# Kernel optimization log

Measured on AMD Instinct MI355X. Metric: run time of the kernel, lower is better.

Reference implementation:

```python
import jax, jax.numpy as jnp
import numpy as np


def _gru_cell(x, h, Wih, Whh, bih, bhh):
    # PyTorch GRU cell (seq_len=1): gates ordered r, z, n
    gi = x @ Wih.T + bih
    gh = h @ Whh.T + bhh
    i_r, i_z, i_n = jnp.split(gi, 3, axis=-1)
    h_r, h_z, h_n = jnp.split(gh, 3, axis=-1)
    r = jax.nn.sigmoid(i_r + h_r)
    z = jax.nn.sigmoid(i_z + h_z)
    n = jnp.tanh(i_n + r * h_n)
    return (1.0 - z) * n + z * h


def setup_inputs() -> dict:
    key = jax.random.key(0)
    N, K, n_in, H = 4096, 8, 14, 128
    ks = jax.random.split(key, 24)
    s = 0.05
    inp = {
        "towers": jax.random.normal(ks[0], (N, K, n_in), jnp.float32),
        # E_n encoder (Linear -> tanh -> Linear -> tanh)
        "En_W1": jax.random.normal(ks[1], (H, n_in)) * s,
        "En_b1": jnp.zeros((H,)),
        "En_W2": jax.random.normal(ks[2], (H, H)) * s,
        "En_b2": jnp.zeros((H,)),
        # E_e encoder
        "Ee_W1": jax.random.normal(ks[3], (H, 2 * n_in)) * s,
        "Ee_b1": jnp.zeros((H,)),
        "Ee_W2": jax.random.normal(ks[4], (H, H)) * s,
        "Ee_b2": jnp.zeros((H,)),
        # U_gru (node update), input n_in + H
        "U_Wih": jax.random.normal(ks[5], (3 * H, n_in + H)) * s,
        "U_Whh": jax.random.normal(ks[6], (3 * H, H)) * s,
        "U_bih": jnp.zeros((3 * H,)),
        "U_bhh": jnp.zeros((3 * H,)),
        # M_gru (edge update), input 2*(n_in + H)
        "M_Wih": jax.random.normal(ks[7], (3 * H, 2 * (n_in + H))) * s,
        "M_Whh": jax.random.normal(ks[8], (3 * H, H)) * s,
        "M_bih": jnp.zeros((3 * H,)),
        "M_bhh": jnp.zeros((3 * H,)),
        # G_gru (global update), input 2*H
        "G_Wih": jax.random.normal(ks[9], (3 * H, 2 * H)) * s,
        "G_Whh": jax.random.normal(ks[10], (3 * H, H)) * s,
        "G_bih": jnp.zeros((3 * H,)),
        "G_bhh": jnp.zeros((3 * H,)),
        # output head
        "O_W": jax.random.normal(ks[11], (1, H)) * s,
        "O_b": jnp.zeros((1,)),
        "k": 3,
    }
    return inp


def reference(towers, En_W1, En_b1, En_W2, En_b2, Ee_W1, Ee_b1, Ee_W2, Ee_b2,
              U_Wih, U_Whh, U_bih, U_bhh, M_Wih, M_Whh, M_bih, M_bhh,
              G_Wih, G_Whh, G_bih, G_bhh, O_W, O_b, k):
    N, K, n_in = towers.shape
    H = En_W1.shape[0]
    # node state init: h = E_n(towers)
    h = jnp.tanh(jnp.tanh(towers @ En_W1.T + En_b1) @ En_W2.T + En_b2)  # (N,K,H)
    # edge state init: e_h = E_e(all-pairs concat of towers)
    xi = jnp.broadcast_to(towers[:, :, None, :], (N, K, K, n_in))
    xj = jnp.broadcast_to(towers[:, None, :, :], (N, K, K, n_in))
    xx0 = jnp.concatenate([xi, xj], axis=-1)  # (N,K,K,2*n_in)
    e_h = jnp.tanh(jnp.tanh(xx0 @ Ee_W1.T + Ee_b1) @ Ee_W2.T + Ee_b2)  # (N,K,K,H)
    # mask[i,j] = 1 iff j == i+1 (the nested-loop mask is a shifted identity)
    mask = jnp.eye(K, k=1, dtype=towers.dtype)
    e = e_h
    D = n_in + H
    for _ in range(k):
        # edge_fn: all-pairs concat of [towers, h] fed through GRU cell
        xh = jnp.concatenate([towers, h], axis=-1)  # (N,K,D)
        a = jnp.broadcast_to(xh[:, :, None, :], (N, K, K, D))
        b = jnp.broadcast_to(xh[:, None, :, :], (N, K, K, D))
        exx = jnp.concatenate([a, b], axis=-1).reshape(-1, 2 * D)
        e_h = _gru_cell(exx, e_h.reshape(-1, H), M_Wih, M_Whh, M_bih, M_bhh)
        e = e_h.reshape(N, K, K, H)
        # node_fn: masked sum selects e[:, i, i+1]
        edges = jnp.einsum('nijh,ij->nih', e, mask)  # (N,K,H)
        nx = jnp.concatenate([towers, edges], axis=-1).reshape(-1, D)
        h = _gru_cell(nx, h.reshape(-1, H), U_Wih, U_Whh, U_bih, U_bhh).reshape(N, K, H)
        e_h = e_h  # state carried
    # global_fn
    h_sum = h.sum(axis=1)  # (N,H)
    e_sum = jnp.einsum('nijh,ij->nh', e, mask)  # (N,H)
    gx = jnp.concatenate([h_sum, e_sum], axis=-1)  # (N,2H)
    g = _gru_cell(gx, jnp.zeros((N, H), towers.dtype), G_Wih, G_Whh, G_bih, G_bhh)
    out = jax.nn.sigmoid((g @ O_W.T + O_b).reshape(N))
    return out
```

## Files before the change

kernel.cpp:

```cpp
#include <hip/hip_runtime.h>
#include <hip/hip_bf16.h>

typedef __hip_bfloat16 bf16;
typedef unsigned short ush;
typedef short s16x8 __attribute__((ext_vector_type(8)));
typedef ush u16x4 __attribute__((ext_vector_type(4)));
typedef float f32x4 __attribute__((ext_vector_type(4)));

#define DEV __device__ __forceinline__

DEV float rcp_f(float x) { return __builtin_amdgcn_rcpf(x); }
DEV float sigmoid_f(float x) { return rcp_f(1.f + __expf(-x)); }
DEV float tanh_f(float x) { return 1.f - 2.f * rcp_f(__expf(2.f * x) + 1.f); }

DEV float u2f(ush u) { unsigned int v = ((unsigned int)u) << 16; float f; __builtin_memcpy(&f, &v, 4); return f; }
DEV ush f2u(float f) { bf16 h = __float2bfloat16(f); ush u; __builtin_memcpy(&u, &h, 2); return u; }

DEV f32x4 MFMA(s16x8 a, s16x8 b, f32x4 c) {
  return __builtin_amdgcn_mfma_f32_16x16x32_bf16(a, b, c, 0, 0, 0);
}

DEV s16x8 z8() {
  s16x8 v;
  for (int z = 0; z < 8; ++z) v[z] = 0;
  return v;
}

DEV int swz_idx(int row, int kk) { return row * 32 + (((kk >> 3) ^ ((row >> 1) & 3)) << 3) + (kk & 7); }
DEV int swz_blk(int row, int blk) { return row * 32 + ((blk ^ ((row >> 1) & 3)) << 3); }


__global__ __launch_bounds__(256) void prep_all(
    const float* __restrict__ towers,
    const float* __restrict__ MWih, const float* __restrict__ MWhh,
    const float* __restrict__ UWih, const float* __restrict__ UWhh,
    const float* __restrict__ EnW1, const float* __restrict__ EnW2,
    const float* __restrict__ EeW1, const float* __restrict__ EeW2,
    const float* __restrict__ MBih, const float* __restrict__ MBhh,
    const float* __restrict__ UBih, const float* __restrict__ UBhh,
    const float* __restrict__ GWih, const float* __restrict__ GWhh,
    const float* __restrict__ GBih, const float* __restrict__ GBhh,
    ush* __restrict__ xh, ush* __restrict__ WPQ, ush* __restrict__ WTh,
    ush* __restrict__ WTu, ush* __restrict__ WBen1, ush* __restrict__ WBen2,
    ush* __restrict__ WBee1, ush* __restrict__ WBee2,
    float* __restrict__ biasM, float* __restrict__ biasU,
    float* __restrict__ WT_G, float* __restrict__ biasG, ush* __restrict__ bn2rep)
{
  const int b = blockIdx.x, t = threadIdx.x;
  if (b < 2048) {
    const int idx = b * 256 + t;
    const int row = idx >> 4, kk = idx & 15;
    xh[row * 144 + kk] = f2u(kk < 14 ? towers[row * 14 + kk] : 0.f);
  } else if (b < 2528) {
    const int idx = (b - 2048) * 256 + t;
    const int ck = idx / 24576, rem = idx % 24576, n = rem >> 5, kk = rem & 31;
    const int k = ck * 32 + kk;
    const int half = (n >= 384);
    const int m = n - half * 384;
    const int g = m >> 7, c = m & 127;
    const int row = g * 128 + c;
    int col = -1;
    if (k < 14)                  col = k;
    else if (k >= 16 && k < 144) col = k - 2;
    if (half && col >= 0)        col += 142;
    WPQ[idx] = f2u((col >= 0) ? MWih[row * 284 + col] : 0.f);
  } else if (b < 2720) {
    const int idx = (b - 2528) * 256 + t;
    const int ck = idx / 12288, rem = idx % 12288, n = rem >> 5, kk = rem & 31;
    const int g = n >> 7, c = n & 127;
    WTh[idx] = f2u(MWhh[(g * 128 + c) * 128 + ck * 32 + kk]);
  } else if (b < 3296) {
    const int idx = (b - 2720) * 256 + t;
    const int ck = idx >> 14, n = (idx >> 5) & 511, kk = idx & 31;
    const int k = ck * 32 + kk, gate = n >> 7, c = n & 127;
    float w = 0.f;
    const int row = (gate == 0) ? c : (gate == 1) ? 128 + c : 256 + c;
    if (k < 160) {
      int col = -1;
      if (k < 16)        { if (k < 14) col = k; }
      else if (k < 144)  col = 14 + (k - 16);
      if (gate != 3 && col >= 0) w = UWih[row * 142 + col];
    } else {
      if (gate != 2) w = UWhh[row * 128 + (k - 160)];
    }
    WTu[ck * 16384 + swz_idx(n, kk)] = f2u(w);
  } else if (b < 3312) {
    const int idx = (b - 3296) * 256 + t;
    const int n = (idx >> 5) & 127, kk = idx & 31;
    WBen1[idx] = f2u(kk < 14 ? EnW1[n * 14 + kk] : 0.f);
  } else if (b < 3376) {
    const int idx = (b - 3312) * 256 + t;
    const int ck = idx >> 12, n = (idx >> 5) & 127, kk = idx & 31;
    WBen2[idx] = f2u(EnW2[n * 128 + ck * 32 + kk]);
  } else if (b < 3392) {
    const int idx = (b - 3376) * 256 + t;
    const int n = (idx >> 5) & 127, kk = idx & 31;
    int col = (kk < 16) ? (kk < 14 ? kk : -1) : (kk < 30 ? 14 + (kk - 16) : -1);
    WBee1[idx] = f2u(col >= 0 ? EeW1[n * 28 + col] : 0.f);
    (void)n;
  } else if (b < 3456) {
    const int idx = (b - 3392) * 256 + t;
    const int ck = idx >> 12, n = (idx >> 5) & 127, kk = idx & 31;
    WBee2[idx] = f2u(EeW2[n * 128 + ck * 32 + kk]);
  } else if (b < 3458) {
    const int idx = (b - 3456) * 256 + t;
    const int g = idx >> 7, c = idx & 127;
    float v;
    if (g == 0)      v = MBih[c] + MBhh[c];
    else if (g == 1) v = MBih[128 + c] + MBhh[128 + c];
    else if (g == 2) v = MBih[256 + c];
    else             v = MBhh[256 + c];
    biasM[idx] = v;
  } else if (b < 3460) {
    const int idx = (b - 3458) * 256 + t;
    const int g = idx >> 7, c = idx & 127;
    float v;
    if (g == 0)      v = UBih[c] + UBhh[c];
    else if (g == 1) v = UBih[128 + c] + UBhh[128 + c];
    else if (g == 2) v = UBih[256 + c];
    else             v = UBhh[256 + c];
    biasU[idx] = v;
  } else if (b < 4228) {
    const int idx = (b - 3460) * 256 + t;
    const int kc = idx >> 9, cg = (idx >> 2) & 127, gate = idx & 3;
    const int row = (gate == 0) ? cg : (gate == 1) ? cg + 128 : cg + 256;
    float v = 0.f;
    if (kc < 256) { if (gate != 3) v = GWih[row * 256 + kc]; }
    else          { if (gate != 2) v = GWhh[row * 128 + (kc - 256)]; }
    WT_G[idx] = v;
  } else if (b < 4230) {
    const int idx = (b - 4228) * 256 + t;
    const int cg = idx >> 2, gate = idx & 3;
    float v;
    if (gate == 0)      v = GBih[cg] + GBhh[cg];
    else if (gate == 1) v = GBih[cg + 128] + GBhh[cg + 128];
    else if (gate == 2) v = GBih[cg + 256];
    else                v = GBhh[cg + 256];
    biasG[idx] = v;
  } else {
    const int idx = (b - 4230) * 256 + t;
    bn2rep[idx] = f2u(MBhh[256 + (idx >> 3)]);
  }
}

DEV void pq_phase(ush* As5, const ush* __restrict__ WPQ,
                  const float* __restrict__ biasM, ush* __restrict__ PqT,
                  int rowBase, int lane, int w)
{
  const int quad = lane >> 4, l15 = lane & 15;
  for (int half = 0; half < 2; ++half) {
    f32x4 acc[6][4];
    #pragma unroll
    for (int tl = 0; tl < 6; ++tl)
      #pragma unroll
      for (int rt = 0; rt < 4; ++rt) {
        #pragma unroll
        for (int q = 0; q < 4; ++q) acc[tl][rt][q] = 0.f;
      }
    for (int ck = 0; ck < 5; ++ck) {
      s16x8 af[4];
      #pragma unroll
      for (int rt = 0; rt < 4; ++rt)
        af[rt] = *(const s16x8*)&As5[ck * 2048 + swz_blk(rt * 16 + l15, quad)];
      #pragma unroll
      for (int tl = 0; tl < 6; ++tl) {
        const int n = w * 96 + tl * 16 + l15;
        const s16x8 bf = *(const s16x8*)&WPQ[(ck * 768 + half * 384 + n) * 32 + quad * 8];
        #pragma unroll
        for (int rt = 0; rt < 4; ++rt) acc[tl][rt] = MFMA(af[rt], bf, acc[tl][rt]);
      }
    }
    #pragma unroll
    for (int tl = 0; tl < 6; ++tl) {
      const int col = w * 96 + tl * 16 + l15;
      const float bv = half ? 0.f : biasM[col];
      #pragma unroll
      for (int rt = 0; rt < 4; ++rt) {
        const int row0 = rowBase + rt * 16 + quad * 4;
        const int g = row0 >> 3, n0 = row0 & 7;
        u16x4 wv;
        #pragma unroll
        for (int q = 0; q < 4; ++q) wv[q] = f2u(acc[tl][rt][q] + bv);
        *(u16x4*)&PqT[((size_t)g * 768 + half * 384 + col) * 8 + n0] = wv;
      }
    }
  }
}

DEV void pq_stage_towers(ush* As5, const ush* __restrict__ xh, int rowBase, int t)
{
  const int gm = t >> 2, gb = t & 3, grow = rowBase + gm;
  if (gb < 2) {
    const s16x8 v = *(const s16x8*)(xh + grow * 144 + gb * 8);
    *(s16x8*)&As5[swz_blk(gm, gb)] = v;
  } else {
    *(s16x8*)&As5[4 * 2048 + swz_blk(gm, gb)] = z8();
  }
}

__global__ __launch_bounds__(256, 2) void enc_en_pq(
    ush* __restrict__ xh,
    const ush* __restrict__ WB1, const float* __restrict__ b1,
    const ush* __restrict__ WB2, const float* __restrict__ b2,
    const ush* __restrict__ WPQ, const float* __restrict__ biasM,
    ush* __restrict__ PqT)
{
  __shared__ ush smem[10240];
  ush* A1  = smem;
  ush* Z1  = smem + 1024;
  ush* As5 = smem;
  const int t = threadIdx.x, lane = t & 63, w = t >> 6;
  const int rowBase = blockIdx.x * 64;
  const int quad = lane >> 4, l15 = lane & 15;

  {
    const int gm = t >> 2, gb = t & 3, grow = rowBase + gm;
    s16x8 v = z8();
    if (gb < 2) v = *(const s16x8*)(xh + grow * 144 + gb * 8);
    *(s16x8*)&A1[swz_blk(gm, gb)] = v;
  }
  __syncthreads();

  s16x8 af[4];
  #pragma unroll
  for (int rt = 0; rt < 4; ++rt)
    af[rt] = *(const s16x8*)&A1[swz_blk(rt * 16 + l15, quad)];
  f32x4 acc1[4][2];
  #pragma unroll
  for (int rt = 0; rt < 4; ++rt)
    #pragma unroll
    for (int ct = 0; ct < 2; ++ct) {
      #pragma unroll
      for (int q = 0; q < 4; ++q) acc1[rt][ct][q] = 0.f;
    }
  #pragma unroll
  for (int ct = 0; ct < 2; ++ct) {
    const int n = w * 32 + ct * 16 + l15;
    const s16x8 bf = *(const s16x8*)&WB1[n * 32 + quad * 8];
    #pragma unroll
    for (int rt = 0; rt < 4; ++rt) acc1[rt][ct] = MFMA(af[rt], bf, acc1[rt][ct]);
  }
  #pragma unroll
  for (int ct = 0; ct < 2; ++ct) {
    const int col = w * 32 + ct * 16 + l15;
    const int kk = col & 31;
    #pragma unroll
    for (int rt = 0; rt < 4; ++rt) {
      #pragma unroll
      for (int q = 0; q < 4; ++q) {
        const int m = rt * 16 + quad * 4 + q;
        Z1[w * 2048 + swz_idx(m, kk)] = f2u(tanh_f(acc1[rt][ct][q] + b1[col]));
      }
    }
  }
  __syncthreads();

  f32x4 acc2[4][2];
  #pragma unroll
  for (int rt = 0; rt < 4; ++rt)
    #pragma unroll
    for (int ct = 0; ct < 2; ++ct) {
      #pragma unroll
      for (int q = 0; q < 4; ++q) acc2[rt][ct][q] = 0.f;
    }
  for (int ck2 = 0; ck2 < 4; ++ck2) {
    #pragma unroll
    for (int rt = 0; rt < 4; ++rt)
      af[rt] = *(const s16x8*)&Z1[ck2 * 2048 + swz_blk(rt * 16 + l15, quad)];
    #pragma unroll
    for (int ct = 0; ct < 2; ++ct) {
      const int n = w * 32 + ct * 16 + l15;
      const s16x8 bf = *(const s16x8*)&WB2[(ck2 * 128 + n) * 32 + quad * 8];
      #pragma unroll
      for (int rt = 0; rt < 4; ++rt) acc2[rt][ct] = MFMA(af[rt], bf, acc2[rt][ct]);
    }
  }
  __syncthreads();

  #pragma unroll
  for (int ct = 0; ct < 2; ++ct) {
    const int col = w * 32 + ct * 16 + l15;
    const int k = 16 + col, ck = k >> 5, kk = k & 31;
    #pragma unroll
    for (int rt = 0; rt < 4; ++rt) {
      #pragma unroll
      for (int q = 0; q < 4; ++q) {
        const int r = rt * 16 + quad * 4 + q;
        const ush hv = f2u(tanh_f(acc2[rt][ct][q] + b2[col]));
        xh[(rowBase + r) * 144 + 16 + col] = hv;
        As5[ck * 2048 + swz_idx(r, kk)] = hv;
      }
    }
  }
  pq_stage_towers(As5, xh, rowBase, t);
  __syncthreads();
  pq_phase(As5, WPQ, biasM, PqT, rowBase, lane, w);
}

DEV void edge_sparse_gru(ush* As, ush* __restrict__ eh,
                         const ush* __restrict__ WTh,
                         const ush* __restrict__ PqT,
                         const ush* __restrict__ bn2rep,
                         int G0, int t)
{
  const int lane = t & 63, w = t >> 6;
  const int quad = lane >> 4, l15 = lane & 15;

  f32x4 accR[2][4], accZ[2][4], accN1[2][4], accN2[2][4];
  #pragma unroll
  for (int mt = 0; mt < 2; ++mt)
    #pragma unroll
    for (int nt = 0; nt < 4; ++nt) {
      #pragma unroll
      for (int q = 0; q < 4; ++q) { accR[mt][nt][q] = 0.f; accZ[mt][nt][q] = 0.f; accN1[mt][nt][q] = 0.f; accN2[mt][nt][q] = 0.f; }
    }

  #pragma unroll
  for (int ck = 0; ck < 4; ++ck) {
    s16x8 be[4];
    #pragma unroll
    for (int nt = 0; nt < 4; ++nt)
      be[nt] = *(const s16x8*)&As[ck * 2048 + swz_blk(nt * 16 + l15, quad)];
    #pragma unroll
    for (int mt = 0; mt < 2; ++mt) {
      const int nb = w * 32 + mt * 16 + l15;
      const int ko = quad * 8;
      const s16x8 aR = *(const s16x8*)&WTh[(ck * 384 + nb) * 32 + ko];
      const s16x8 aZ = *(const s16x8*)&WTh[(ck * 384 + 128 + nb) * 32 + ko];
      const s16x8 aN = *(const s16x8*)&WTh[(ck * 384 + 256 + nb) * 32 + ko];
      #pragma unroll
      for (int nt = 0; nt < 4; ++nt) {
        accR[mt][nt]  = MFMA(aR, be[nt], accR[mt][nt]);
        accZ[mt][nt]  = MFMA(aZ, be[nt], accZ[mt][nt]);
        accN2[mt][nt] = MFMA(aN, be[nt], accN2[mt][nt]);
      }
    }
  }

  {
    s16x8 bI = z8();
    const int i0 = l15 & 7, hi = l15 >> 3;
    if (quad == hi)                       bI[i0]     = (short)0x3F80;
    else if (quad == 2 + hi && i0 < 7)    bI[i0 + 1] = (short)0x3F80;
    const int part = quad >> 1;
    #pragma unroll
    for (int p = 0; p < 4; ++p) {
      const ush* base = PqT + ((size_t)(G0 + 2 * p + (quad & 1)) * 768 + part * 384) * 8;
      #pragma unroll
      for (int mt = 0; mt < 2; ++mt) {
        const int c = w * 32 + mt * 16 + l15;
        const s16x8 aR  = *(const s16x8*)&base[(c) * 8];
        const s16x8 aZ  = *(const s16x8*)&base[(128 + c) * 8];
        const s16x8 aN1 = *(const s16x8*)&base[(256 + c) * 8];
        s16x8 aN2 = z8();
        if (part == 0) aN2 = *(const s16x8*)&bn2rep[c * 8];
        accR[mt][p]  = MFMA(aR,  bI, accR[mt][p]);
        accZ[mt][p]  = MFMA(aZ,  bI, accZ[mt][p]);
        accN1[mt][p] = MFMA(aN1, bI, accN1[mt][p]);
        accN2[mt][p] = MFMA(aN2, bI, accN2[mt][p]);
      }
    }
  }

  #pragma unroll
  for (int mt = 0; mt < 2; ++mt) {
    const int hc0 = w * 32 + mt * 16 + quad * 4;
    const int ck2 = hc0 >> 5, kkB = hc0 & 31;
    #pragma unroll
    for (int nt = 0; nt < 4; ++nt) {
      const int erow = nt * 16 + l15;
      const int gg = erow >> 3, i = erow & 7;
      if (i == 7) continue;
      const u16x4 hp4 = *(const u16x4*)&As[ck2 * 2048 + swz_blk(erow, kkB >> 3) + (kkB & 7)];
      u16x4 ov;
      #pragma unroll
      for (int q = 0; q < 4; ++q) {
        const float rg = sigmoid_f(accR[mt][nt][q]);
        const float zg = sigmoid_f(accZ[mt][nt][q]);
        const float nn = tanh_f(accN1[mt][nt][q] + rg * accN2[mt][nt][q]);
        const float hp = u2f(hp4[q]);
        ov[q] = f2u(nn + zg * (hp - nn));
      }
      *(u16x4*)&eh[(size_t)((G0 + gg) * 64 + i * 9 + 1) * 128 + hc0] = ov;
    }
  }
}

__global__ __launch_bounds__(256, 2) void edge_first(
    ush* __restrict__ eh, const ush* __restrict__ WTh,
    const ush* __restrict__ PqT, const ush* __restrict__ bn2rep,
    const ush* __restrict__ xh,
    const ush* __restrict__ WB1, const float* __restrict__ b1,
    const ush* __restrict__ WB2, const float* __restrict__ b2)
{
  __shared__ ush smem[17408];
  ush* As = smem;
  ush* A1 = smem + 8192;
  ush* Z1 = smem + 9216;
  const int t = threadIdx.x, lane = t & 63, w = t >> 6;
  const int G0 = blockIdx.x * 8;
  const int quad = lane >> 4, l15 = lane & 15;

  {
    const int gm = t >> 2, gb = t & 3;
    const int gg = gm >> 3, i = gm & 7;
    const int xi = (G0 + gg) * 8 + i;
    const int xj = (i < 7) ? xi + 1 : xi;
    const s16x8 v = (gb < 2) ? *(const s16x8*)(xh + xi * 144 + gb * 8)
                             : *(const s16x8*)(xh + xj * 144 + (gb - 2) * 8);
    *(s16x8*)&A1[swz_blk(gm, gb)] = v;
  }
  __syncthreads();

  s16x8 af[4];
  #pragma unroll
  for (int rt = 0; rt < 4; ++rt)
    af[rt] = *(const s16x8*)&A1[swz_blk(rt * 16 + l15, quad)];
  f32x4 acc1[4][2];
  #pragma unroll
  for (int rt = 0; rt < 4; ++rt)
    #pragma unroll
    for (int ct = 0; ct < 2; ++ct) {
      #pragma unroll
      for (int q = 0; q < 4; ++q) acc1[rt][ct][q] = 0.f;
    }
  #pragma unroll
  for (int ct = 0; ct < 2; ++ct) {
    const int n = w * 32 + ct * 16 + l15;
    const s16x8 bf = *(const s16x8*)&WB1[n * 32 + quad * 8];
    #pragma unroll
    for (int rt = 0; rt < 4; ++rt) acc1[rt][ct] = MFMA(af[rt], bf, acc1[rt][ct]);
  }
  #pragma unroll
  for (int ct = 0; ct < 2; ++ct) {
    const int col = w * 32 + ct * 16 + l15;
    const int kk = col & 31;
    #pragma unroll
    for (int rt = 0; rt < 4; ++rt) {
      #pragma unroll
      for (int q = 0; q < 4; ++q) {
        const int m = rt * 16 + quad * 4 + q;
        Z1[w * 2048 + swz_idx(m, kk)] = f2u(tanh_f(acc1[rt][ct][q] + b1[col]));
      }
    }
  }
  __syncthreads();

  f32x4 acc2[4][2];
  #pragma unroll
  for (int rt = 0; rt < 4; ++rt)
    #pragma unroll
    for (int ct = 0; ct < 2; ++ct) {
      #pragma unroll
      for (int q = 0; q < 4; ++q) acc2[rt][ct][q] = 0.f;
    }
  for (int ck2 = 0; ck2 < 4; ++ck2) {
    #pragma unroll
    for (int rt = 0; rt < 4; ++rt)
      af[rt] = *(const s16x8*)&Z1[ck2 * 2048 + swz_blk(rt * 16 + l15, quad)];
    #pragma unroll
    for (int ct = 0; ct < 2; ++ct) {
      const int n = w * 32 + ct * 16 + l15;
      const s16x8 bf = *(const s16x8*)&WB2[(ck2 * 128 + n) * 32 + quad * 8];
      #pragma unroll
      for (int rt = 0; rt < 4; ++rt) acc2[rt][ct] = MFMA(af[rt], bf, acc2[rt][ct]);
    }
  }
  #pragma unroll
  for (int ct = 0; ct < 2; ++ct) {
    const int col = w * 32 + ct * 16 + l15;
    const int kk = col & 31;
    #pragma unroll
    for (int rt = 0; rt < 4; ++rt) {
      #pragma unroll
      for (int q = 0; q < 4; ++q) {
        const int r = rt * 16 + quad * 4 + q;
        As[(col >> 5) * 2048 + swz_idx(r, kk)] = f2u(tanh_f(acc2[rt][ct][q] + b2[col]));
      }
    }
  }
  __syncthreads();

  edge_sparse_gru(As, eh, WTh, PqT, bn2rep, G0, t);
}

__global__ __launch_bounds__(256, 2) void edge_last(
    ush* __restrict__ eh, const ush* __restrict__ WTh,
    const ush* __restrict__ PqT, const ush* __restrict__ bn2rep)
{
  __shared__ ush As[8192];
  const int t = threadIdx.x;
  const int G0 = blockIdx.x * 8;

  {
    const int gm = t >> 2, gb = t & 3;
    const int gg = gm >> 3, i = gm & 7;
    const ush* src = eh + (size_t)((G0 + gg) * 64 + i * 9 + 1) * 128;
    #pragma unroll
    for (int ck = 0; ck < 4; ++ck) {
      s16x8 v = z8();
      if (i < 7) v = *(const s16x8*)(src + ck * 32 + gb * 8);
      *(s16x8*)&As[ck * 2048 + swz_blk(gm, gb)] = v;
    }
  }
  __syncthreads();

  edge_sparse_gru(As, eh, WTh, PqT, bn2rep, G0, t);
}

template<int PQ>
__global__ __launch_bounds__(256, 2) void gru_node_pq(
    ush* __restrict__ xh, const ush* __restrict__ eh,
    const ush* __restrict__ WT, const float* __restrict__ bias,
    const ush* __restrict__ WPQ, const float* __restrict__ biasM,
    ush* __restrict__ PqT)
{
  constexpr int NCH = 9, XCH = 5;
  __shared__ ush smem[10240];
  ush* As5 = smem;
  const int t = threadIdx.x, lane = t & 63, w = t >> 6;
  const int rowBase = blockIdx.x * 64;
  const int gm = t >> 2, gb = t & 3, grow = rowBase + gm;
  const int l15 = lane & 15, quad = lane >> 4;

  f32x4 accR[4][2], accZ[4][2], accN1[4][2], accN2[4][2];
  #pragma unroll
  for (int rt = 0; rt < 4; ++rt)
    #pragma unroll
    for (int s = 0; s < 2; ++s) {
      #pragma unroll
      for (int q = 0; q < 4; ++q) { accR[rt][s][q] = 0.f; accZ[rt][s][q] = 0.f; accN1[rt][s][q] = 0.f; accN2[rt][s][q] = 0.f; }
    }

  auto stage = [&](int ck) {
    const int k0 = ck * 32 + gb * 8;
    s16x8 v = z8();
    if (k0 < 16)       v = *(const s16x8*)(xh + grow * 144 + k0);
    else if (k0 < 144) {
      const int i = grow & 7;
      if (i < 7) v = *(const s16x8*)(eh + (size_t)(grow * 8 + i + 1) * 128 + (k0 - 16));
    } else if (k0 >= 160) {
      v = *(const s16x8*)(xh + grow * 144 + 16 + (k0 - 160));
    }
    *(s16x8*)&smem[(ck & 1) * 2048 + swz_blk(gm, gb)] = v;
  };

  stage(0);
  __syncthreads();

  for (int ck = 0; ck < NCH; ++ck) {
    if (ck + 1 < NCH) stage(ck + 1);

    const ush* Wc = WT + ck * 16384;
    const ush* Ac = smem + (ck & 1) * 2048;
    s16x8 af[4];
    #pragma unroll
    for (int rt = 0; rt < 4; ++rt)
      af[rt] = *(const s16x8*)&Ac[swz_blk(rt * 16 + l15, quad)];
    if (ck < XCH) {
      #pragma unroll
      for (int s = 0; s < 2; ++s) {
        const int nb = w * 32 + s * 16 + l15;
        const s16x8 bR = *(const s16x8*)&Wc[swz_blk(0 * 128 + nb, quad)];
        const s16x8 bZ = *(const s16x8*)&Wc[swz_blk(1 * 128 + nb, quad)];
        const s16x8 bN = *(const s16x8*)&Wc[swz_blk(2 * 128 + nb, quad)];
        #pragma unroll
        for (int rt = 0; rt < 4; ++rt) {
          accR[rt][s]  = MFMA(af[rt], bR, accR[rt][s]);
          accZ[rt][s]  = MFMA(af[rt], bZ, accZ[rt][s]);
          accN1[rt][s] = MFMA(af[rt], bN, accN1[rt][s]);
        }
      }
    } else {
      #pragma unroll
      for (int s = 0; s < 2; ++s) {
        const int nb = w * 32 + s * 16 + l15;
        const s16x8 bR = *(const s16x8*)&Wc[swz_blk(0 * 128 + nb, quad)];
        const s16x8 bZ = *(const s16x8*)&Wc[swz_blk(1 * 128 + nb, quad)];
        const s16x8 bN = *(const s16x8*)&Wc[swz_blk(3 * 128 + nb, quad)];
        #pragma unroll
        for (int rt = 0; rt < 4; ++rt) {
          accR[rt][s]  = MFMA(af[rt], bR, accR[rt][s]);
          accZ[rt][s]  = MFMA(af[rt], bZ, accZ[rt][s]);
          accN2[rt][s] = MFMA(af[rt], bN, accN2[rt][s]);
        }
      }
    }
    __syncthreads();
  }

  #pragma unroll
  for (int s = 0; s < 2; ++s) {
    const int hcol = w * 32 + s * 16 + l15;
    const float bR = bias[hcol], bZ = bias[128 + hcol], bN1 = bias[256 + hcol], bN2 = bias[384 + hcol];
    const int k = 16 + hcol, ckh = k >> 5, kkh = k & 31;
    #pragma unroll
    for (int rt = 0; rt < 4; ++rt) {
      #pragma unroll
      for (int q = 0; q < 4; ++q) {
        const int r = rt * 16 + quad * 4 + q;
        const int row = rowBase + r;
        const float hp = u2f(xh[row * 144 + 16 + hcol]);
        const float rg = sigmoid_f(accR[rt][s][q] + bR);
        const float zg = sigmoid_f(accZ[rt][s][q] + bZ);
        const float nn = tanh_f(accN1[rt][s][q] + bN1 + rg * (accN2[rt][s][q] + bN2));
        const ush hv = f2u(nn + zg * (hp - nn));
        xh[row * 144 + 16 + hcol] = hv;
        if (PQ) As5[ckh * 2048 + swz_idx(r, kkh)] = hv;
      }
    }
  }
  if (PQ) {
    pq_stage_towers(As5, xh, rowBase, t);
    __syncthreads();
    pq_phase(As5, WPQ, biasM, PqT, rowBase, lane, w);
  }
}

__global__ __launch_bounds__(256) void sums2(const ush* __restrict__ xh, const ush* __restrict__ eh,
                                             float* __restrict__ hsum, float* __restrict__ esum) {
  const int idx = blockIdx.x * 256 + threadIdx.x;
  const int n = idx >> 7, hh = idx & 127;
  float hs = 0.f, es = 0.f;
  #pragma unroll
  for (int i = 0; i < 8; ++i) hs += u2f(xh[(n * 8 + i) * 144 + 16 + hh]);
  #pragma unroll
  for (int i = 0; i < 7; ++i) es += u2f(eh[(size_t)((n * 8 + i) * 8 + i + 1) * 128 + hh]);
  hsum[idx] = hs;
  esum[idx] = es;
}

__global__ __launch_bounds__(256) void gru_global_out(
    const float* __restrict__ hsum, const float* __restrict__ esum,
    const float* __restrict__ WT, const float* __restrict__ bias,
    const float* __restrict__ OW, const float* __restrict__ Ob,
    float* __restrict__ out)
{
  constexpr int KT = 384;
  __shared__ float4 ATl4[KT * 4];
  __shared__ float4 Bl4[16 * 128];
  __shared__ float gmat[16 * 128];
  __shared__ float red[16 * 4];
  float* ATl = (float*)ATl4;
  const int t = threadIdx.x;
  const int rowBase = blockIdx.x * 16;
  for (int idx = t; idx < KT * 16; idx += 256) {
    const int kc = idx >> 4, r = idx & 15, grow = rowBase + r;
    float v = 0.f;
    if (kc < 128)      v = hsum[grow * 128 + kc];
    else if (kc < 256) v = esum[grow * 128 + (kc - 128)];
    ATl[idx] = v;
  }
  const int c = t & 127, rh = t >> 7;
  float accR[8], accZ[8], accN1[8];
  #pragma unroll
  for (int rr = 0; rr < 8; ++rr) { accR[rr] = 0.f; accZ[rr] = 0.f; accN1[rr] = 0.f; }
  const float4* WT4 = (const float4*)WT;
  for (int ck = 0; ck < 16; ++ck) {
    __syncthreads();
    #pragma unroll
    for (int ii = 0; ii < 8; ++ii) { const int idx = t + ii * 256; Bl4[idx] = WT4[ck * 2048 + idx]; }
    __syncthreads();
    const int kb = ck * 16;
    #pragma unroll
    for (int kcl = 0; kcl < 16; ++kcl) {
      const float4 wv = Bl4[kcl * 128 + c];
      const float4 a0 = ATl4[(kb + kcl) * 4 + rh * 2];
      const float4 a1 = ATl4[(kb + kcl) * 4 + rh * 2 + 1];
      const float av[8] = {a0.x, a0.y, a0.z, a0.w, a1.x, a1.y, a1.z, a1.w};
      #pragma unroll
      for (int rr = 0; rr < 8; ++rr) {
        accR[rr]  += wv.x * av[rr];
        accZ[rr]  += wv.y * av[rr];
        accN1[rr] += wv.z * av[rr];
      }
    }
  }
  const float4 bb = ((const float4*)bias)[c];
  const float ow = OW[c];
  #pragma unroll
  for (int rr = 0; rr < 8; ++rr) {
    const float rg = sigmoid_f(accR[rr] + bb.x);
    const float zg = sigmoid_f(accZ[rr] + bb.y);
    const float nn = tanh_f(accN1[rr] + bb.z + rg * bb.w);
    gmat[(rh * 8 + rr) * 128 + c] = (1.f - zg) * nn * ow;
  }
  __syncthreads();
  if (t < 64) {
    const int r = t >> 2, part = t & 3;
    float s = 0.f;
    #pragma unroll
    for (int cc = 0; cc < 32; ++cc) s += gmat[r * 128 + part * 32 + cc];
    red[r * 4 + part] = s;
  }
  __syncthreads();
  if (t < 16) {
    const float s = red[t * 4] + red[t * 4 + 1] + red[t * 4 + 2] + red[t * 4 + 3];
    out[rowBase + t] = sigmoid_f(s + Ob[0]);
  }
}

extern "C" void kernel_launch(void* const* d_in, const int* in_sizes, int n_in,
                              void* d_out, int out_size, void* d_ws, size_t ws_size,
                              hipStream_t stream)
{
  (void)in_sizes; (void)n_in; (void)out_size; (void)ws_size;
  const float* towers = (const float*)d_in[0];
  const float* EnW1 = (const float*)d_in[1];
  const float* EnB1 = (const float*)d_in[2];
  const float* EnW2 = (const float*)d_in[3];
  const float* EnB2 = (const float*)d_in[4];
  const float* EeW1 = (const float*)d_in[5];
  const float* EeB1 = (const float*)d_in[6];
  const float* EeW2 = (const float*)d_in[7];
  const float* EeB2 = (const float*)d_in[8];
  const float* UWih = (const float*)d_in[9];
  const float* UWhh = (const float*)d_in[10];
  const float* UBih = (const float*)d_in[11];
  const float* UBhh = (const float*)d_in[12];
  const float* MWih = (const float*)d_in[13];
  const float* MWhh = (const float*)d_in[14];
  const float* MBih = (const float*)d_in[15];
  const float* MBhh = (const float*)d_in[16];
  const float* GWih = (const float*)d_in[17];
  const float* GWhh = (const float*)d_in[18];
  const float* GBih = (const float*)d_in[19];
  const float* GBhh = (const float*)d_in[20];
  const float* OW   = (const float*)d_in[21];
  const float* Ob   = (const float*)d_in[22];

  char* ws = (char*)d_ws;
  size_t off = 0;
  auto take = [&](size_t b) { void* p = ws + off; off = (off + b + 255) & ~(size_t)255; return p; };
  ush*   xh     = (ush*)take((size_t)32768 * 144 * 2);
  ush*   eh     = (ush*)take((size_t)262144 * 128 * 2);
  ush*   PqT    = (ush*)take((size_t)4096 * 768 * 8 * 2);
  float* hsum   = (float*)take((size_t)4096 * 128 * 4);
  float* esum   = (float*)take((size_t)4096 * 128 * 4);
  ush*   WPQ    = (ush*)take((size_t)5 * 768 * 32 * 2);
  ush*   WTh    = (ush*)take((size_t)4 * 384 * 32 * 2);
  ush*   WTu    = (ush*)take((size_t)9 * 512 * 32 * 2);
  ush*   WBen1  = (ush*)take((size_t)128 * 32 * 2);
  ush*   WBen2  = (ush*)take((size_t)4 * 128 * 32 * 2);
  ush*   WBee1  = (ush*)take((size_t)128 * 32 * 2);
  ush*   WBee2  = (ush*)take((size_t)4 * 128 * 32 * 2);
  float* biasM  = (float*)take(512 * 4);
  float* biasU  = (float*)take(512 * 4);
  float* WT_G   = (float*)take((size_t)384 * 512 * 4);
  float* biasG  = (float*)take(512 * 4);
  ush*   bn2rep = (ush*)take(128 * 8 * 2);

  prep_all<<<4234, 256, 0, stream>>>(
      towers, MWih, MWhh, UWih, UWhh, EnW1, EnW2, EeW1, EeW2,
      MBih, MBhh, UBih, UBhh, GWih, GWhh, GBih, GBhh,
      xh, WPQ, WTh, WTu, WBen1, WBen2, WBee1, WBee2,
      biasM, biasU, WT_G, biasG, bn2rep);

  enc_en_pq<<<512, 256, 0, stream>>>(xh, WBen1, EnB1, WBen2, EnB2, WPQ, biasM, PqT);

  edge_first<<<512, 256, 0, stream>>>(eh, WTh, PqT, bn2rep, xh, WBee1, EeB1, WBee2, EeB2);
  gru_node_pq<1><<<512, 256, 0, stream>>>(xh, eh, WTu, biasU, WPQ, biasM, PqT);
  edge_last<<<512, 256, 0, stream>>>(eh, WTh, PqT, bn2rep);
  gru_node_pq<1><<<512, 256, 0, stream>>>(xh, eh, WTu, biasU, WPQ, biasM, PqT);
  edge_last<<<512, 256, 0, stream>>>(eh, WTh, PqT, bn2rep);
  gru_node_pq<0><<<512, 256, 0, stream>>>(xh, eh, WTu, biasU, WPQ, biasM, PqT);

  sums2<<<2048, 256, 0, stream>>>(xh, eh, hsum, esum);
  gru_global_out<<<256, 256, 0, stream>>>(hsum, esum, WT_G, biasG, OW, Ob, (float*)d_out);
}
```

Before: 295.4 us.

## Compute edge input projection directly per edge instead of precomputed P/Q node tables

Drops the factored per-node P/Q projection tables (PqT) that were built in the encoder and node kernels and then combined through identity-MFMA gathers in the edge kernel. Each edge kernel now stages the concatenated [xh_i, xh_{i+1}] rows into shared memory with double buffering and multiplies them by a full 288-wide input weight matrix, with biases applied in the epilogue. This removes the PqT global round-trip and the pq_phase from the node kernels, and shrinks their shared-memory use. In exchange the edge kernel does more MFMA work, roughly 9 K-chunks instead of the old identity gather, and adds a barrier per chunk.

```diff
diff --git a/kernel.cpp b/kernel.cpp
--- a/kernel.cpp
+++ b/kernel.cpp
@@ -40,37 +40,36 @@
     const float* __restrict__ UBih, const float* __restrict__ UBhh,
     const float* __restrict__ GWih, const float* __restrict__ GWhh,
     const float* __restrict__ GBih, const float* __restrict__ GBhh,
-    ush* __restrict__ xh, ush* __restrict__ WPQ, ush* __restrict__ WTh,
+    ush* __restrict__ xh, ush* __restrict__ WIHe, ush* __restrict__ WTh,
     ush* __restrict__ WTu, ush* __restrict__ WBen1, ush* __restrict__ WBen2,
     ush* __restrict__ WBee1, ush* __restrict__ WBee2,
     float* __restrict__ biasM, float* __restrict__ biasU,
-    float* __restrict__ WT_G, float* __restrict__ biasG, ush* __restrict__ bn2rep)
+    float* __restrict__ WT_G, float* __restrict__ biasG)
 {
   const int b = blockIdx.x, t = threadIdx.x;
   if (b < 2048) {
     const int idx = b * 256 + t;
     const int row = idx >> 4, kk = idx & 15;
     xh[row * 144 + kk] = f2u(kk < 14 ? towers[row * 14 + kk] : 0.f);
-  } else if (b < 2528) {
+  } else if (b < 2480) {
     const int idx = (b - 2048) * 256 + t;
-    const int ck = idx / 24576, rem = idx % 24576, n = rem >> 5, kk = rem & 31;
+    const int ck = idx / 12288, rem = idx % 12288, n = rem >> 5, kk = rem & 31;
     const int k = ck * 32 + kk;
-    const int half = (n >= 384);
-    const int m = n - half * 384;
-    const int g = m >> 7, c = m & 127;
-    const int row = g * 128 + c;
+    const int gate = n >> 7, c = n & 127;
+    const int row = gate * 128 + c;
     int col = -1;
-    if (k < 14)                  col = k;
-    else if (k >= 16 && k < 144) col = k - 2;
-    if (half && col >= 0)        col += 142;
-    WPQ[idx] = f2u((col >= 0) ? MWih[row * 284 + col] : 0.f);
-  } else if (b < 2720) {
-    const int idx = (b - 2528) * 256 + t;
+    if (k < 14)                    col = k;
+    else if (k >= 16 && k < 144)   col = 14 + (k - 16);
+    else if (k >= 144 && k < 158)  col = 142 + (k - 144);
+    else if (k >= 160)             col = 156 + (k - 160);
+    WIHe[idx] = f2u((col >= 0) ? MWih[row * 284 + col] : 0.f);
+  } else if (b < 2672) {
+    const int idx = (b - 2480) * 256 + t;
     const int ck = idx / 12288, rem = idx % 12288, n = rem >> 5, kk = rem & 31;
     const int g = n >> 7, c = n & 127;
     WTh[idx] = f2u(MWhh[(g * 128 + c) * 128 + ck * 32 + kk]);
-  } else if (b < 3296) {
-    const int idx = (b - 2720) * 256 + t;
+  } else if (b < 3248) {
+    const int idx = (b - 2672) * 256 + t;
     const int ck = idx >> 14, n = (idx >> 5) & 511, kk = idx & 31;
     const int k = ck * 32 + kk, gate = n >> 7, c = n & 127;
     float w = 0.f;
@@ -84,26 +83,26 @@
       if (gate != 2) w = UWhh[row * 128 + (k - 160)];
     }
     WTu[ck * 16384 + swz_idx(n, kk)] = f2u(w);
-  } else if (b < 3312) {
-    const int idx = (b - 3296) * 256 + t;
+  } else if (b < 3264) {
+    const int idx = (b - 3248) * 256 + t;
     const int n = (idx >> 5) & 127, kk = idx & 31;
     WBen1[idx] = f2u(kk < 14 ? EnW1[n * 14 + kk] : 0.f);
-  } else if (b < 3376) {
-    const int idx = (b - 3312) * 256 + t;
+  } else if (b < 3328) {
+    const int idx = (b - 3264) * 256 + t;
     const int ck = idx >> 12, n = (idx >> 5) & 127, kk = idx & 31;
     WBen2[idx] = f2u(EnW2[n * 128 + ck * 32 + kk]);
-  } else if (b < 3392) {
-    const int idx = (b - 3376) * 256 + t;
+  } else if (b < 3344) {
+    const int idx = (b - 3328) * 256 + t;
     const int n = (idx >> 5) & 127, kk = idx & 31;
     int col = (kk < 16) ? (kk < 14 ? kk : -1) : (kk < 30 ? 14 + (kk - 16) : -1);
     WBee1[idx] = f2u(col >= 0 ? EeW1[n * 28 + col] : 0.f);
     (void)n;
-  } else if (b < 3456) {
-    const int idx = (b - 3392) * 256 + t;
+  } else if (b < 3408) {
+    const int idx = (b - 3344) * 256 + t;
     const int ck = idx >> 12, n = (idx >> 5) & 127, kk = idx & 31;
     WBee2[idx] = f2u(EeW2[n * 128 + ck * 32 + kk]);
-  } else if (b < 3458) {
-    const int idx = (b - 3456) * 256 + t;
+  } else if (b < 3410) {
+    const int idx = (b - 3408) * 256 + t;
     const int g = idx >> 7, c = idx & 127;
     float v;
     if (g == 0)      v = MBih[c] + MBhh[c];
@@ -111,8 +110,8 @@
     else if (g == 2) v = MBih[256 + c];
     else             v = MBhh[256 + c];
     biasM[idx] = v;
-  } else if (b < 3460) {
-    const int idx = (b - 3458) * 256 + t;
+  } else if (b < 3412) {
+    const int idx = (b - 3410) * 256 + t;
     const int g = idx >> 7, c = idx & 127;
     float v;
     if (g == 0)      v = UBih[c] + UBhh[c];
@@ -120,16 +119,16 @@
     else if (g == 2) v = UBih[256 + c];
     else             v = UBhh[256 + c];
     biasU[idx] = v;
-  } else if (b < 4228) {
-    const int idx = (b - 3460) * 256 + t;
+  } else if (b < 4180) {
+    const int idx = (b - 3412) * 256 + t;
     const int kc = idx >> 9, cg = (idx >> 2) & 127, gate = idx & 3;
     const int row = (gate == 0) ? cg : (gate == 1) ? cg + 128 : cg + 256;
     float v = 0.f;
     if (kc < 256) { if (gate != 3) v = GWih[row * 256 + kc]; }
     else          { if (gate != 2) v = GWhh[row * 128 + (kc - 256)]; }
     WT_G[idx] = v;
-  } else if (b < 4230) {
-    const int idx = (b - 4228) * 256 + t;
+  } else {
+    const int idx = (b - 4180) * 256 + t;
     const int cg = idx >> 2, gate = idx & 3;
     float v;
     if (gate == 0)      v = GBih[cg] + GBhh[cg];
@@ -137,78 +136,17 @@
     else if (gate == 2) v = GBih[cg + 256];
     else                v = GBhh[cg + 256];
     biasG[idx] = v;
-  } else {
-    const int idx = (b - 4230) * 256 + t;
-    bn2rep[idx] = f2u(MBhh[256 + (idx >> 3)]);
-  }
-}
-
-DEV void pq_phase(ush* As5, const ush* __restrict__ WPQ,
-                  const float* __restrict__ biasM, ush* __restrict__ PqT,
-                  int rowBase, int lane, int w)
-{
-  const int quad = lane >> 4, l15 = lane & 15;
-  for (int half = 0; half < 2; ++half) {
-    f32x4 acc[6][4];
-    #pragma unroll
-    for (int tl = 0; tl < 6; ++tl)
-      #pragma unroll
-      for (int rt = 0; rt < 4; ++rt) {
-        #pragma unroll
-        for (int q = 0; q < 4; ++q) acc[tl][rt][q] = 0.f;
-      }
-    for (int ck = 0; ck < 5; ++ck) {
-      s16x8 af[4];
-      #pragma unroll
-      for (int rt = 0; rt < 4; ++rt)
-        af[rt] = *(const s16x8*)&As5[ck * 2048 + swz_blk(rt * 16 + l15, quad)];
-      #pragma unroll
-      for (int tl = 0; tl < 6; ++tl) {
-        const int n = w * 96 + tl * 16 + l15;
-        const s16x8 bf = *(const s16x8*)&WPQ[(ck * 768 + half * 384 + n) * 32 + quad * 8];
-        #pragma unroll
-        for (int rt = 0; rt < 4; ++rt) acc[tl][rt] = MFMA(af[rt], bf, acc[tl][rt]);
-      }
-    }
-    #pragma unroll
-    for (int tl = 0; tl < 6; ++tl) {
-      const int col = w * 96 + tl * 16 + l15;
-      const float bv = half ? 0.f : biasM[col];
-      #pragma unroll
-      for (int rt = 0; rt < 4; ++rt) {
-        const int row0 = rowBase + rt * 16 + quad * 4;
-        const int g = row0 >> 3, n0 = row0 & 7;
-        u16x4 wv;
-        #pragma unroll
-        for (int q = 0; q < 4; ++q) wv[q] = f2u(acc[tl][rt][q] + bv);
-        *(u16x4*)&PqT[((size_t)g * 768 + half * 384 + col) * 8 + n0] = wv;
-      }
-    }
-  }
-}
-
-DEV void pq_stage_towers(ush* As5, const ush* __restrict__ xh, int rowBase, int t)
-{
-  const int gm = t >> 2, gb = t & 3, grow = rowBase + gm;
-  if (gb < 2) {
-    const s16x8 v = *(const s16x8*)(xh + grow * 144 + gb * 8);
-    *(s16x8*)&As5[swz_blk(gm, gb)] = v;
-  } else {
-    *(s16x8*)&As5[4 * 2048 + swz_blk(gm, gb)] = z8();
-  }
-}
-
-__global__ __launch_bounds__(256, 2) void enc_en_pq(
+  }
+}
+
+__global__ __launch_bounds__(256, 2) void enc_en(
     ush* __restrict__ xh,
     const ush* __restrict__ WB1, const float* __restrict__ b1,
-    const ush* __restrict__ WB2, const float* __restrict__ b2,
-    const ush* __restrict__ WPQ, const float* __restrict__ biasM,
-    ush* __restrict__ PqT)
-{
-  __shared__ ush smem[10240];
-  ush* A1  = smem;
-  ush* Z1  = smem + 1024;
-  ush* As5 = smem;
+    const ush* __restrict__ WB2, const float* __restrict__ b2)
+{
+  __shared__ ush smem[9216];
+  ush* A1 = smem;
+  ush* Z1 = smem + 1024;
   const int t = threadIdx.x, lane = t & 63, w = t >> 6;
   const int rowBase = blockIdx.x * 64;
   const int quad = lane >> 4, l15 = lane & 15;
@@ -275,130 +213,29 @@
       for (int rt = 0; rt < 4; ++rt) acc2[rt][ct] = MFMA(af[rt], bf, acc2[rt][ct]);
     }
   }
-  __syncthreads();
 
   #pragma unroll
   for (int ct = 0; ct < 2; ++ct) {
     const int col = w * 32 + ct * 16 + l15;
-    const int k = 16 + col, ck = k >> 5, kk = k & 31;
     #pragma unroll
     for (int rt = 0; rt < 4; ++rt) {
       #pragma unroll
       for (int q = 0; q < 4; ++q) {
         const int r = rt * 16 + quad * 4 + q;
-        const ush hv = f2u(tanh_f(acc2[rt][ct][q] + b2[col]));
-        xh[(rowBase + r) * 144 + 16 + col] = hv;
-        As5[ck * 2048 + swz_idx(r, kk)] = hv;
-      }
-    }
-  }
-  pq_stage_towers(As5, xh, rowBase, t);
-  __syncthreads();
-  pq_phase(As5, WPQ, biasM, PqT, rowBase, lane, w);
-}
-
-DEV void edge_sparse_gru(ush* As, ush* __restrict__ eh,
-                         const ush* __restrict__ WTh,
-                         const ush* __restrict__ PqT,
-                         const ush* __restrict__ bn2rep,
-                         int G0, int t)
-{
+        xh[(rowBase + r) * 144 + 16 + col] = f2u(tanh_f(acc2[rt][ct][q] + b2[col]));
+      }
+    }
+  }
+}
+
+DEV void ee_body(ush* As_e, ush* SC, const ush* __restrict__ xh,
+                 const ush* __restrict__ WB1, const float* __restrict__ b1,
+                 const ush* __restrict__ WB2, const float* __restrict__ b2,
+                 int G0, int t)
+{
+  ush* A1 = SC;
+  ush* Z1 = SC + 1024;
   const int lane = t & 63, w = t >> 6;
-  const int quad = lane >> 4, l15 = lane & 15;
-
-  f32x4 accR[2][4], accZ[2][4], accN1[2][4], accN2[2][4];
-  #pragma unroll
-  for (int mt = 0; mt < 2; ++mt)
-    #pragma unroll
-    for (int nt = 0; nt < 4; ++nt) {
-      #pragma unroll
-      for (int q = 0; q < 4; ++q) { accR[mt][nt][q] = 0.f; accZ[mt][nt][q] = 0.f; accN1[mt][nt][q] = 0.f; accN2[mt][nt][q] = 0.f; }
-    }
-
-  #pragma unroll
-  for (int ck = 0; ck < 4; ++ck) {
-    s16x8 be[4];
-    #pragma unroll
-    for (int nt = 0; nt < 4; ++nt)
-      be[nt] = *(const s16x8*)&As[ck * 2048 + swz_blk(nt * 16 + l15, quad)];
-    #pragma unroll
-    for (int mt = 0; mt < 2; ++mt) {
-      const int nb = w * 32 + mt * 16 + l15;
-      const int ko = quad * 8;
-      const s16x8 aR = *(const s16x8*)&WTh[(ck * 384 + nb) * 32 + ko];
-      const s16x8 aZ = *(const s16x8*)&WTh[(ck * 384 + 128 + nb) * 32 + ko];
-      const s16x8 aN = *(const s16x8*)&WTh[(ck * 384 + 256 + nb) * 32 + ko];
-      #pragma unroll
-      for (int nt = 0; nt < 4; ++nt) {
-        accR[mt][nt]  = MFMA(aR, be[nt], accR[mt][nt]);
-        accZ[mt][nt]  = MFMA(aZ, be[nt], accZ[mt][nt]);
-        accN2[mt][nt] = MFMA(aN, be[nt], accN2[mt][nt]);
-      }
-    }
-  }
-
-  {
-    s16x8 bI = z8();
-    const int i0 = l15 & 7, hi = l15 >> 3;
-    if (quad == hi)                       bI[i0]     = (short)0x3F80;
-    else if (quad == 2 + hi && i0 < 7)    bI[i0 + 1] = (short)0x3F80;
-    const int part = quad >> 1;
-    #pragma unroll
-    for (int p = 0; p < 4; ++p) {
-      const ush* base = PqT + ((size_t)(G0 + 2 * p + (quad & 1)) * 768 + part * 384) * 8;
-      #pragma unroll
-      for (int mt = 0; mt < 2; ++mt) {
-        const int c = w * 32 + mt * 16 + l15;
-        const s16x8 aR  = *(const s16x8*)&base[(c) * 8];
-        const s16x8 aZ  = *(const s16x8*)&base[(128 + c) * 8];
-        const s16x8 aN1 = *(const s16x8*)&base[(256 + c) * 8];
-        s16x8 aN2 = z8();
-        if (part == 0) aN2 = *(const s16x8*)&bn2rep[c * 8];
-        accR[mt][p]  = MFMA(aR,  bI, accR[mt][p]);
-        accZ[mt][p]  = MFMA(aZ,  bI, accZ[mt][p]);
-        accN1[mt][p] = MFMA(aN1, bI, accN1[mt][p]);
-        accN2[mt][p] = MFMA(aN2, bI, accN2[mt][p]);
-      }
-    }
-  }
-
-  #pragma unroll
-  for (int mt = 0; mt < 2; ++mt) {
-    const int hc0 = w * 32 + mt * 16 + quad * 4;
-    const int ck2 = hc0 >> 5, kkB = hc0 & 31;
-    #pragma unroll
-    for (int nt = 0; nt < 4; ++nt) {
-      const int erow = nt * 16 + l15;
-      const int gg = erow >> 3, i = erow & 7;
-      if (i == 7) continue;
-      const u16x4 hp4 = *(const u16x4*)&As[ck2 * 2048 + swz_blk(erow, kkB >> 3) + (kkB & 7)];
-      u16x4 ov;
-      #pragma unroll
-      for (int q = 0; q < 4; ++q) {
-        const float rg = sigmoid_f(accR[mt][nt][q]);
-        const float zg = sigmoid_f(accZ[mt][nt][q]);
-        const float nn = tanh_f(accN1[mt][nt][q] + rg * accN2[mt][nt][q]);
-        const float hp = u2f(hp4[q]);
-        ov[q] = f2u(nn + zg * (hp - nn));
-      }
-      *(u16x4*)&eh[(size_t)((G0 + gg) * 64 + i * 9 + 1) * 128 + hc0] = ov;
-    }
-  }
-}
-
-__global__ __launch_bounds__(256, 2) void edge_first(
-    ush* __restrict__ eh, const ush* __restrict__ WTh,
-    const ush* __restrict__ PqT, const ush* __restrict__ bn2rep,
-    const ush* __restrict__ xh,
-    const ush* __restrict__ WB1, const float* __restrict__ b1,
-    const ush* __restrict__ WB2, const float* __restrict__ b2)
-{
-  __shared__ ush smem[17408];
-  ush* As = smem;
-  ush* A1 = smem + 8192;
-  ush* Z1 = smem + 9216;
-  const int t = threadIdx.x, lane = t & 63, w = t >> 6;
-  const int G0 = blockIdx.x * 8;
   const int quad = lane >> 4, l15 = lane & 15;
 
   {
@@ -475,20 +312,139 @@
       #pragma unroll
       for (int q = 0; q < 4; ++q) {
         const int r = rt * 16 + quad * 4 + q;
-        As[(col >> 5) * 2048 + swz_idx(r, kk)] = f2u(tanh_f(acc2[rt][ct][q] + b2[col]));
-      }
-    }
-  }
-  __syncthreads();
-
-  edge_sparse_gru(As, eh, WTh, PqT, bn2rep, G0, t);
-}
-
-__global__ __launch_bounds__(256, 2) void edge_last(
-    ush* __restrict__ eh, const ush* __restrict__ WTh,
-    const ush* __restrict__ PqT, const ush* __restrict__ bn2rep)
-{
-  __shared__ ush As[8192];
+        As_e[(col >> 5) * 2048 + swz_idx(r, kk)] = f2u(tanh_f(acc2[rt][ct][q] + b2[col]));
+      }
+    }
+  }
+}
+
+DEV void edge_gru_core(const ush* As_e, ush* Bxx, ush* __restrict__ eh,
+                       const ush* __restrict__ WIHe, const ush* __restrict__ WTh,
+                       const float* __restrict__ biasM,
+                       const ush* __restrict__ xh, int G0, int t)
+{
+  const int lane = t & 63, w = t >> 6;
+  const int quad = lane >> 4, l15 = lane & 15;
+  const int ko = quad * 8;
+
+  f32x4 accR[2][4], accZ[2][4], accN1[2][4], accN2[2][4];
+  #pragma unroll
+  for (int mt = 0; mt < 2; ++mt)
+    #pragma unroll
+    for (int nt = 0; nt < 4; ++nt) {
+      #pragma unroll
+      for (int q = 0; q < 4; ++q) { accR[mt][nt][q] = 0.f; accZ[mt][nt][q] = 0.f; accN1[mt][nt][q] = 0.f; accN2[mt][nt][q] = 0.f; }
+    }
+
+  auto stage_xx = [&](int ck) {
+    const int gm = t >> 2, gb = t & 3;
+    const int gg = gm >> 3, i = gm & 7;
+    const int xi = (G0 + gg) * 8 + i;
+    const int xj = xi + ((i < 7) ? 1 : 0);
+    const int k0 = ck * 32 + gb * 8;
+    const s16x8 v = (k0 < 144) ? *(const s16x8*)(xh + xi * 144 + k0)
+                               : *(const s16x8*)(xh + xj * 144 + (k0 - 144));
+    *(s16x8*)&Bxx[(ck & 1) * 2048 + swz_blk(gm, gb)] = v;
+  };
+
+  stage_xx(0);
+  __syncthreads();
+  for (int ck = 0; ck < 9; ++ck) {
+    if (ck + 1 < 9) stage_xx(ck + 1);
+    const ush* Bc = Bxx + (ck & 1) * 2048;
+    s16x8 be[4];
+    #pragma unroll
+    for (int nt = 0; nt < 4; ++nt)
+      be[nt] = *(const s16x8*)&Bc[swz_blk(nt * 16 + l15, quad)];
+    #pragma unroll
+    for (int mt = 0; mt < 2; ++mt) {
+      const int nb = w * 32 + mt * 16 + l15;
+      const s16x8 aR = *(const s16x8*)&WIHe[(ck * 384 + nb) * 32 + ko];
+      const s16x8 aZ = *(const s16x8*)&WIHe[(ck * 384 + 128 + nb) * 32 + ko];
+      const s16x8 aN = *(const s16x8*)&WIHe[(ck * 384 + 256 + nb) * 32 + ko];
+      #pragma unroll
+      for (int nt = 0; nt < 4; ++nt) {
+        accR[mt][nt]  = MFMA(aR, be[nt], accR[mt][nt]);
+        accZ[mt][nt]  = MFMA(aZ, be[nt], accZ[mt][nt]);
+        accN1[mt][nt] = MFMA(aN, be[nt], accN1[mt][nt]);
+      }
+    }
+    __syncthreads();
+  }
+
+  #pragma unroll
+  for (int ck = 0; ck < 4; ++ck) {
+    s16x8 be[4];
+    #pragma unroll
+    for (int nt = 0; nt < 4; ++nt)
+      be[nt] = *(const s16x8*)&As_e[ck * 2048 + swz_blk(nt * 16 + l15, quad)];
+    #pragma unroll
+    for (int mt = 0; mt < 2; ++mt) {
+      const int nb = w * 32 + mt * 16 + l15;
+      const s16x8 aR = *(const s16x8*)&WTh[(ck * 384 + nb) * 32 + ko];
+      const s16x8 aZ = *(const s16x8*)&WTh[(ck * 384 + 128 + nb) * 32 + ko];
+      const s16x8 aN = *(const s16x8*)&WTh[(ck * 384 + 256 + nb) * 32 + ko];
+      #pragma unroll
+      for (int nt = 0; nt < 4; ++nt) {
+        accR[mt][nt]  = MFMA(aR, be[nt], accR[mt][nt]);
+        accZ[mt][nt]  = MFMA(aZ, be[nt], accZ[mt][nt]);
+        accN2[mt][nt] = MFMA(aN, be[nt], accN2[mt][nt]);
+      }
+    }
+  }
+
+  #pragma unroll
+  for (int mt = 0; mt < 2; ++mt) {
+    const int hc0 = w * 32 + mt * 16 + quad * 4;
+    const int ck2 = hc0 >> 5, kkB = hc0 & 31;
+    #pragma unroll
+    for (int nt = 0; nt < 4; ++nt) {
+      const int erow = nt * 16 + l15;
+      const int gg = erow >> 3, i = erow & 7;
+      if (i == 7) continue;
+      const u16x4 hp4 = *(const u16x4*)&As_e[ck2 * 2048 + swz_blk(erow, kkB >> 3) + (kkB & 7)];
+      u16x4 ov;
+      #pragma unroll
+      for (int q = 0; q < 4; ++q) {
+        const int c = hc0 + q;
+        const float rg = sigmoid_f(accR[mt][nt][q] + biasM[c]);
+        const float zg = sigmoid_f(accZ[mt][nt][q] + biasM[128 + c]);
+        const float nn = tanh_f(accN1[mt][nt][q] + biasM[256 + c]
+                                + rg * (accN2[mt][nt][q] + biasM[384 + c]));
+        const float hp = u2f(hp4[q]);
+        ov[q] = f2u(nn + zg * (hp - nn));
+      }
+      *(u16x4*)&eh[(size_t)((G0 + gg) * 64 + i * 9 + 1) * 128 + hc0] = ov;
+    }
+  }
+}
+
+__global__ __launch_bounds__(256, 2) void edge_first(
+    ush* __restrict__ eh, const ush* __restrict__ WIHe,
+    const ush* __restrict__ WTh, const float* __restrict__ biasM,
+    const ush* __restrict__ xh,
+    const ush* __restrict__ WB1, const float* __restrict__ b1,
+    const ush* __restrict__ WB2, const float* __restrict__ b2)
+{
+  __shared__ ush smem[17408];
+  ush* As_e = smem;
+  ush* SC   = smem + 8192;
+  const int t = threadIdx.x;
+  const int G0 = blockIdx.x * 8;
+
+  ee_body(As_e, SC, xh, WB1, b1, WB2, b2, G0, t);
+  __syncthreads();
+  edge_gru_core(As_e, SC, eh, WIHe, WTh, biasM, xh, G0, t);
+}
+
+__global__ __launch_bounds__(256, 2) void edge_next(
+    ush* __restrict__ eh, const ush* __restrict__ WIHe,
+    const ush* __restrict__ WTh, const float* __restrict__ biasM,
+    const ush* __restrict__ xh)
+{
+  __shared__ ush smem[12288];
+  ush* As_e = smem;
+  ush* Bxx  = smem + 8192;
   const int t = threadIdx.x;
   const int G0 = blockIdx.x * 8;
 
@@ -500,24 +456,20 @@
     for (int ck = 0; ck < 4; ++ck) {
       s16x8 v = z8();
       if (i < 7) v = *(const s16x8*)(src + ck * 32 + gb * 8);
-      *(s16x8*)&As[ck * 2048 + swz_blk(gm, gb)] = v;
-    }
-  }
-  __syncthreads();
-
-  edge_sparse_gru(As, eh, WTh, PqT, bn2rep, G0, t);
-}
-
-template<int PQ>
-__global__ __launch_bounds__(256, 2) void gru_node_pq(
+      *(s16x8*)&As_e[ck * 2048 + swz_blk(gm, gb)] = v;
+    }
+  }
+  __syncthreads();
+
+  edge_gru_core(As_e, Bxx, eh, WIHe, WTh, biasM, xh, G0, t);
+}
+
+__global__ __launch_bounds__(256, 2) void gru_node(
     ush* __restrict__ xh, const ush* __restrict__ eh,
-    const ush* __restrict__ WT, const float* __restrict__ bias,
-    const ush* __restrict__ WPQ, const float* __restrict__ biasM,
-    ush* __restrict__ PqT)
+    const ush* __restrict__ WT, const float* __restrict__ bias)
 {
   constexpr int NCH = 9, XCH = 5;
-  __shared__ ush smem[10240];
-  ush* As5 = smem;
+  __shared__ ush smem[4096];
   const int t = threadIdx.x, lane = t & 63, w = t >> 6;
   const int rowBase = blockIdx.x * 64;
   const int gm = t >> 2, gb = t & 3, grow = rowBase + gm;
@@ -593,7 +545,6 @@
   for (int s = 0; s < 2; ++s) {
     const int hcol = w * 32 + s * 16 + l15;
     const float bR = bias[hcol], bZ = bias[128 + hcol], bN1 = bias[256 + hcol], bN2 = bias[384 + hcol];
-    const int k = 16 + hcol, ckh = k >> 5, kkh = k & 31;
     #pragma unroll
     for (int rt = 0; rt < 4; ++rt) {
       #pragma unroll
@@ -604,16 +555,9 @@
         const float rg = sigmoid_f(accR[rt][s][q] + bR);
         const float zg = sigmoid_f(accZ[rt][s][q] + bZ);
         const float nn = tanh_f(accN1[rt][s][q] + bN1 + rg * (accN2[rt][s][q] + bN2));
-        const ush hv = f2u(nn + zg * (hp - nn));
-        xh[row * 144 + 16 + hcol] = hv;
-        if (PQ) As5[ckh * 2048 + swz_idx(r, kkh)] = hv;
-      }
-    }
-  }
-  if (PQ) {
-    pq_stage_towers(As5, xh, rowBase, t);
-    __syncthreads();
-    pq_phase(As5, WPQ, biasM, PqT, rowBase, lane, w);
+        xh[row * 144 + 16 + hcol] = f2u(nn + zg * (hp - nn));
+      }
+    }
   }
 }
 
@@ -734,10 +678,9 @@
   auto take = [&](size_t b) { void* p = ws + off; off = (off + b + 255) & ~(size_t)255; return p; };
   ush*   xh     = (ush*)take((size_t)32768 * 144 * 2);
   ush*   eh     = (ush*)take((size_t)262144 * 128 * 2);
-  ush*   PqT    = (ush*)take((size_t)4096 * 768 * 8 * 2);
   float* hsum   = (float*)take((size_t)4096 * 128 * 4);
   float* esum   = (float*)take((size_t)4096 * 128 * 4);
-  ush*   WPQ    = (ush*)take((size_t)5 * 768 * 32 * 2);
+  ush*   WIHe   = (ush*)take((size_t)9 * 384 * 32 * 2);
   ush*   WTh    = (ush*)take((size_t)4 * 384 * 32 * 2);
   ush*   WTu    = (ush*)take((size_t)9 * 512 * 32 * 2);
   ush*   WBen1  = (ush*)take((size_t)128 * 32 * 2);
@@ -748,22 +691,21 @@
   float* biasU  = (float*)take(512 * 4);
   float* WT_G   = (float*)take((size_t)384 * 512 * 4);
   float* biasG  = (float*)take(512 * 4);
-  ush*   bn2rep = (ush*)take(128 * 8 * 2);
-
-  prep_all<<<4234, 256, 0, stream>>>(
+
+  prep_all<<<4182, 256, 0, stream>>>(
       towers, MWih, MWhh, UWih, UWhh, EnW1, EnW2, EeW1, EeW2,
       MBih, MBhh, UBih, UBhh, GWih, GWhh, GBih, GBhh,
-      xh, WPQ, WTh, WTu, WBen1, WBen2, WBee1, WBee2,
-      biasM, biasU, WT_G, biasG, bn2rep);
-
-  enc_en_pq<<<512, 256, 0, stream>>>(xh, WBen1, EnB1, WBen2, EnB2, WPQ, biasM, PqT);
-
-  edge_first<<<512, 256, 0, stream>>>(eh, WTh, PqT, bn2rep, xh, WBee1, EeB1, WBee2, EeB2);
-  gru_node_pq<1><<<512, 256, 0, stream>>>(xh, eh, WTu, biasU, WPQ, biasM, PqT);
-  edge_last<<<512, 256, 0, stream>>>(eh, WTh, PqT, bn2rep);
-  gru_node_pq<1><<<512, 256, 0, stream>>>(xh, eh, WTu, biasU, WPQ, biasM, PqT);
-  edge_last<<<512, 256, 0, stream>>>(eh, WTh, PqT, bn2rep);
-  gru_node_pq<0><<<512, 256, 0, stream>>>(xh, eh, WTu, biasU, WPQ, biasM, PqT);
+      xh, WIHe, WTh, WTu, WBen1, WBen2, WBee1, WBee2,
+      biasM, biasU, WT_G, biasG);
+
+  enc_en<<<512, 256, 0, stream>>>(xh, WBen1, EnB1, WBen2, EnB2);
+
+  edge_first<<<512, 256, 0, stream>>>(eh, WIHe, WTh, biasM, xh, WBee1, EeB1, WBee2, EeB2);
+  gru_node<<<512, 256, 0, stream>>>(xh, eh, WTu, biasU);
+  edge_next<<<512, 256, 0, stream>>>(eh, WIHe, WTh, biasM, xh);
+  gru_node<<<512, 256, 0, stream>>>(xh, eh, WTu, biasU);
+  edge_next<<<512, 256, 0, stream>>>(eh, WIHe, WTh, biasM, xh);
+  gru_node<<<512, 256, 0, stream>>>(xh, eh, WTu, biasU);
 
   sums2<<<2048, 256, 0, stream>>>(xh, eh, hsum, esum);
   gru_global_out<<<256, 256, 0, stream>>>(hsum, esum, WT_G, biasG, OW, Ob, (float*)d_out);
```

After: 257.8 us. 1.15x faster.
